# Kernel optimization log

Hardware: AMD Instinct MI355X
Metric: run time of the kernel (lower is better)

Reference implementation:

```python
import jax, jax.numpy as jnp
import numpy as np

B, T, S, E, H = 2, 2048, 2048, 1024, 16
DH = E // H

def setup_inputs() -> dict:
    key = jax.random.key(0)
    ks = jax.random.split(key, 12)
    sc = 1.0 / np.sqrt(E)
    inp = {
        'query': jax.random.normal(ks[0], (B, T, E), jnp.float32),
        'key':   jax.random.normal(ks[1], (B, S, E), jnp.float32),
        'value': jax.random.normal(ks[2], (B, S, E), jnp.float32),
        'Wq': jax.random.normal(ks[3], (E, E), jnp.float32) * sc,
        'bq': jnp.zeros((E,), jnp.float32),
        'Wk': jax.random.normal(ks[4], (E, E), jnp.float32) * sc,
        'bk': jnp.zeros((E,), jnp.float32),
        'Wv': jax.random.normal(ks[5], (E, E), jnp.float32) * sc,
        'bv': jnp.zeros((E,), jnp.float32),
        'Wo': jax.random.normal(ks[6], (E, E), jnp.float32) * sc,
        'bo': jnp.zeros((E,), jnp.float32),
    }
    return inp

def reference(query, key, value, Wq, bq, Wk, bk, Wv, bv, Wo, bo):
    # Linear projections (torch nn.Linear: x @ W.T + b)
    Q = query @ Wq.T + bq          # [B,T,E]
    K = key   @ Wk.T + bk          # [B,S,E]
    V = value @ Wv.T + bv          # [B,S,E]
    # split heads -> [B,H,L,DH]
    Q = Q.reshape(B, T, H, DH).transpose(0, 2, 1, 3)
    K = K.reshape(B, S, H, DH).transpose(0, 2, 1, 3)
    V = V.reshape(B, S, H, DH).transpose(0, 2, 1, 3)
    scores = jnp.einsum('bhtd,bhsd->bhts', Q, K) / jnp.sqrt(jnp.float32(DH))
    attn = jax.nn.softmax(scores, axis=-1)            # [B,H,T,S]
    out = jnp.einsum('bhts,bhsd->bhtd', attn, V)      # [B,H,T,DH]
    out = out.transpose(0, 2, 1, 3).reshape(B, T, E)
    out = out @ Wo.T + bo                             # [B,T,E]
    attn_avg = attn.mean(axis=1)                      # average_attn_weights=True
    return out, attn_avg
```

## Files before the change

kernel.cpp:

```cpp
#include <hip/hip_runtime.h>

#define DEV __device__ __forceinline__

typedef __attribute__((ext_vector_type(8))) short short8;
typedef __attribute__((ext_vector_type(4))) float floatx4;
typedef __attribute__((ext_vector_type(2))) unsigned int uint2v;
typedef unsigned short u16;

DEV u16 f2bf(float f) {
  unsigned int u = __float_as_uint(f);
  u += 0x7fffu + ((u >> 16) & 1u);
  return (u16)(u >> 16);
}

DEV unsigned int pk2bf(float a, float b) {
  unsigned int ua = __float_as_uint(a) + 0x8000u;
  unsigned int ub = __float_as_uint(b) + 0x8000u;
  return (ua >> 16) | (ub & 0xffff0000u);
}

DEV void load16_to_lds(const void* g, void* l) {
  __builtin_amdgcn_global_load_lds(
      (const __attribute__((address_space(1))) unsigned int*)g,
      (__attribute__((address_space(3))) unsigned int*)l, 16, 0, 0);
}

#define MFMA16(A, B, C) __builtin_amdgcn_mfma_f32_16x16x32_bf16(A, B, C, 0, 0, 0)

#define QSCALE 0.18033688011112042f

DEV void stage_block(const u16* src_row0, int k0, int ln, void* ldsbase) {
  int r = ln >> 2;
  int p = ((ln & 3) - (ln >> 4)) & 3;
  load16_to_lds((const char*)(src_row0 + (size_t)r * 1024 + k0) + p * 16, ldsbase);
}
DEV const short8* frag_addr(const u16* base, int blk, int c, int q) {
  int slot = c * 4 + ((q + (c >> 2)) & 3);
  return (const short8*)(base + blk * 512 + slot * 8);
}

__global__ __launch_bounds__(256) void cvt_all(
    const float* __restrict__ w0, const float* __restrict__ w1,
    const float* __restrict__ w2, const float* __restrict__ w3,
    const float* __restrict__ a0, const float* __restrict__ a1, const float* __restrict__ a2,
    u16* __restrict__ e0, u16* __restrict__ e1, u16* __restrict__ e2, u16* __restrict__ e3,
    u16* __restrict__ f0, u16* __restrict__ f1, u16* __restrict__ f2) {
  const int t = blockIdx.y;
  const float* s;
  u16* d;
  size_t base;
  if (t < 4) {
    s = t == 0 ? w0 : t == 1 ? w1 : t == 2 ? w2 : w3;
    d = t == 0 ? e0 : t == 1 ? e1 : t == 2 ? e2 : e3;
    base = 0;
  } else {
    int a = (t - 4) >> 2;
    s = a == 0 ? a0 : a == 1 ? a1 : a2;
    d = a == 0 ? f0 : a == 1 ? f1 : f2;
    base = (size_t)((t - 4) & 3) * 1048576;
  }
  size_t i = base + (size_t)(blockIdx.x * 256 + threadIdx.x) * 4;
  float4 v = *(const float4*)(s + i);
  ushort4 o;
  o.x = f2bf(v.x); o.y = f2bf(v.y); o.z = f2bf(v.z); o.w = f2bf(v.w);
  *(ushort4*)(d + i) = o;
}

__global__ __launch_bounds__(256) void qkv_gemm(
    const u16* __restrict__ qb, const u16* __restrict__ kb, const u16* __restrict__ vb,
    const u16* __restrict__ wq, const u16* __restrict__ wk, const u16* __restrict__ wv,
    const float* __restrict__ bq, const float* __restrict__ bk, const float* __restrict__ bv,
    u16* __restrict__ Qh, u16* __restrict__ Kh, u16* __restrict__ VT) {
  __shared__ __align__(16) u16 As[4096];
  __shared__ __align__(16) u16 Bs[4096];
  const int tid = threadIdx.x;
  const int w = tid >> 6, ln = tid & 63, q = ln >> 4, c = ln & 15;
  const int wr = w >> 1, wc = w & 1;
  const int z = blockIdx.z;
  const int m0 = (z == 2 ? blockIdx.x : blockIdx.y) * 128;
  const int n0 = (z == 2 ? blockIdx.y : blockIdx.x) * 128;
  const u16* Asrc = z == 0 ? qb : (z == 1 ? kb : wv);
  const u16* Bsrc = z == 0 ? wq : (z == 1 ? wk : vb);

  floatx4 acc[4][4];
#pragma unroll
  for (int i = 0; i < 4; ++i)
#pragma unroll
    for (int j = 0; j < 4; ++j) acc[i][j] = (floatx4){0.f, 0.f, 0.f, 0.f};

  for (int k0 = 0; k0 < 1024; k0 += 32) {
#pragma unroll
    for (int it = 0; it < 2; ++it) {
      int I = w * 2 + it;
      stage_block(Asrc + (size_t)(m0 + I * 16) * 1024, k0, ln, (char*)As + I * 1024);
      stage_block(Bsrc + (size_t)(n0 + I * 16) * 1024, k0, ln, (char*)Bs + I * 1024);
    }
    __syncthreads();
    short8 a[4], bb[4];
#pragma unroll
    for (int mt = 0; mt < 4; ++mt) a[mt] = *frag_addr(As, wr * 4 + mt, c, q);
#pragma unroll
    for (int nt = 0; nt < 4; ++nt) bb[nt] = *frag_addr(Bs, wc * 4 + nt, c, q);
#pragma unroll
    for (int mt = 0; mt < 4; ++mt)
#pragma unroll
      for (int nt = 0; nt < 4; ++nt) acc[mt][nt] = MFMA16(a[mt], bb[nt], acc[mt][nt]);
    __syncthreads();
  }

  if (z <= 1) {
    const float* bias = z ? bk : bq;
    u16* dst = z ? Kh : Qh;
    const float scale = z ? 1.0f : QSCALE;
    float bn[4];
#pragma unroll
    for (int nt = 0; nt < 4; ++nt) bn[nt] = bias[n0 + wc * 64 + nt * 16 + c];
#pragma unroll
    for (int mt = 0; mt < 4; ++mt)
#pragma unroll
      for (int r = 0; r < 4; ++r) {
        int m = m0 + wr * 64 + mt * 16 + 4 * q + r;
        int bbv = m >> 11, t = m & 2047;
#pragma unroll
        for (int nt = 0; nt < 4; ++nt) {
          int n = n0 + wc * 64 + nt * 16 + c;
          dst[((size_t)(bbv * 16 + (n >> 6)) * 2048 + t) * 64 + (n & 63)] =
              f2bf((acc[mt][nt][r] + bn[nt]) * scale);
        }
      }
  } else {
    float bm[4][4];
#pragma unroll
    for (int mt = 0; mt < 4; ++mt)
#pragma unroll
      for (int r = 0; r < 4; ++r) bm[mt][r] = bv[m0 + wr * 64 + mt * 16 + 4 * q + r];
#pragma unroll
    for (int mt = 0; mt < 4; ++mt)
#pragma unroll
      for (int r = 0; r < 4; ++r) {
        int d = m0 + wr * 64 + mt * 16 + 4 * q + r;
        int hh = d >> 6, dl = d & 63;
#pragma unroll
        for (int nt = 0; nt < 4; ++nt) {
          int s = n0 + wc * 64 + nt * 16 + c;
          int bbv = s >> 11, sl = s & 2047;
          VT[((size_t)(bbv * 16 + hh) * 64 + dl) * 2048 + sl] = f2bf(acc[mt][nt][r] + bm[mt][r]);
        }
      }
  }
}

__global__ __launch_bounds__(256) void oproj_gemm(const u16* __restrict__ Ap, const u16* __restrict__ Wp,
                                                  const float* __restrict__ bias, float* __restrict__ out) {
  __shared__ __align__(16) u16 As[4096];
  __shared__ __align__(16) u16 Bs[2048];
  const int tid = threadIdx.x;
  const int w = tid >> 6, ln = tid & 63, q = ln >> 4, c = ln & 15;
  const int wr = w >> 1, wc = w & 1;
  const int n0 = blockIdx.x * 64, m0 = blockIdx.y * 128;

  floatx4 acc[4][2];
#pragma unroll
  for (int i = 0; i < 4; ++i)
#pragma unroll
    for (int j = 0; j < 2; ++j) acc[i][j] = (floatx4){0.f, 0.f, 0.f, 0.f};

  for (int k0 = 0; k0 < 1024; k0 += 32) {
#pragma unroll
    for (int j = 0; j < 3; ++j) {
      int idx = w * 3 + j;
      if (idx < 8) {
        stage_block(Ap + (size_t)(m0 + idx * 16) * 1024, k0, ln, (char*)As + idx * 1024);
      } else {
        int bi = idx - 8;
        stage_block(Wp + (size_t)(n0 + bi * 16) * 1024, k0, ln, (char*)Bs + bi * 1024);
      }
    }
    __syncthreads();
    short8 a[4], bb[2];
#pragma unroll
    for (int mt = 0; mt < 4; ++mt) a[mt] = *frag_addr(As, wr * 4 + mt, c, q);
#pragma unroll
    for (int nt = 0; nt < 2; ++nt) bb[nt] = *frag_addr(Bs, wc * 2 + nt, c, q);
#pragma unroll
    for (int mt = 0; mt < 4; ++mt)
#pragma unroll
      for (int nt = 0; nt < 2; ++nt) acc[mt][nt] = MFMA16(a[mt], bb[nt], acc[mt][nt]);
    __syncthreads();
  }

  float bn[2];
#pragma unroll
  for (int nt = 0; nt < 2; ++nt) bn[nt] = bias[n0 + wc * 32 + nt * 16 + c];
#pragma unroll
  for (int mt = 0; mt < 4; ++mt)
#pragma unroll
    for (int r = 0; r < 4; ++r) {
      int m = m0 + wr * 64 + mt * 16 + 4 * q + r;
#pragma unroll
      for (int nt = 0; nt < 2; ++nt)
        out[(size_t)m * 1024 + n0 + wc * 32 + nt * 16 + c] = acc[mt][nt][r] + bn[nt];
    }
}

__global__ __launch_bounds__(256) void flash_attn(const u16* __restrict__ Qh, const u16* __restrict__ Kh,
                                                  const u16* __restrict__ VhT, u16* __restrict__ Obuf,
                                                  float* __restrict__ l_ws) {
  __shared__ __align__(16) u16 Ks[4096];
  __shared__ __align__(16) u16 VTs[4096];
  __shared__ __align__(16) u16 Ps[4][2][1152];
  const int tid = threadIdx.x;
  const int w = tid >> 6, ln = tid & 63, q = ln >> 4, c = ln & 15;
  const int t0 = blockIdx.x * 128, h = blockIdx.y, b = blockIdx.z;
  const size_t bh = (size_t)(b * 16 + h);
  const u16* Qbase = Qh + bh * 131072;
  const u16* Kbase = Kh + bh * 131072;
  const u16* Vbase = VhT + bh * 131072;

  short8 qf[2][2];
#pragma unroll
  for (int blk = 0; blk < 2; ++blk) {
    const u16* qr = Qbase + (size_t)(t0 + w * 32 + blk * 16 + c) * 64 + q * 8;
    qf[blk][0] = *(const short8*)qr;
    qf[blk][1] = *(const short8*)(qr + 32);
  }
  floatx4 oacc[2][4];
  float lacc[2] = {0.f, 0.f};
#pragma unroll
  for (int i = 0; i < 2; ++i)
#pragma unroll
    for (int j = 0; j < 4; ++j) oacc[i][j] = (floatx4){0.f, 0.f, 0.f, 0.f};

  const int srow = ln >> 3;
  const int sch = (ln & 7) ^ srow;
  const int cx = c & 7;

  for (int s0 = 0; s0 < 2048; s0 += 64) {
#pragma unroll
    for (int it = 0; it < 2; ++it) {
      int I = w * 2 + it;
      int row = I * 8 + srow;
      load16_to_lds((const char*)Kbase + ((size_t)(s0 + row) * 64 + sch * 8) * 2, (char*)Ks + I * 1024);
      load16_to_lds((const char*)Vbase + ((size_t)row * 2048 + s0 + sch * 8) * 2, (char*)VTs + I * 1024);
    }
    __syncthreads();
#pragma unroll
    for (int st = 0; st < 4; ++st) {
      const int row = st * 16 + c;
      short8 k0 = *(const short8*)(Ks + row * 64 + ((q ^ cx) << 3));
      short8 k1 = *(const short8*)(Ks + row * 64 + (((4 + q) ^ cx) << 3));
#pragma unroll
      for (int blk = 0; blk < 2; ++blk) {
        floatx4 zz = (floatx4){0.f, 0.f, 0.f, 0.f};
        zz = MFMA16(k0, qf[blk][0], zz);
        zz = MFMA16(k1, qf[blk][1], zz);
        float e0 = exp2f(zz[0]), e1 = exp2f(zz[1]), e2 = exp2f(zz[2]), e3 = exp2f(zz[3]);
        lacc[blk] += (e0 + e1) + (e2 + e3);
        uint2v pk = {pk2bf(e0, e1), pk2bf(e2, e3)};
        *(uint2v*)(&Ps[w][blk][c * 72 + st * 16 + 4 * q]) = pk;
      }
    }
    short8 pf[2][2];
#pragma unroll
    for (int blk = 0; blk < 2; ++blk) {
      pf[blk][0] = *(const short8*)(&Ps[w][blk][c * 72 + q * 8]);
      pf[blk][1] = *(const short8*)(&Ps[w][blk][c * 72 + 32 + q * 8]);
    }
#pragma unroll
    for (int dt = 0; dt < 4; ++dt) {
      const int row = dt * 16 + c;
      short8 v0 = *(const short8*)(VTs + row * 64 + ((q ^ cx) << 3));
      short8 v1 = *(const short8*)(VTs + row * 64 + (((4 + q) ^ cx) << 3));
#pragma unroll
      for (int blk = 0; blk < 2; ++blk) {
        oacc[blk][dt] = MFMA16(pf[blk][0], v0, oacc[blk][dt]);
        oacc[blk][dt] = MFMA16(pf[blk][1], v1, oacc[blk][dt]);
      }
    }
    __syncthreads();
  }
#pragma unroll
  for (int blk = 0; blk < 2; ++blk) {
    float v = lacc[blk];
    v += __shfl_xor(v, 16);
    v += __shfl_xor(v, 32);
    lacc[blk] = v;
    if (q == 0) l_ws[bh * 2048 + t0 + w * 32 + blk * 16 + c] = v;
  }
#pragma unroll
  for (int blk = 0; blk < 2; ++blk)
#pragma unroll
    for (int r = 0; r < 4; ++r) {
      float lv = __shfl(lacc[blk], 4 * q + r);
      float inv = __builtin_amdgcn_rcpf(lv);
      const int t = t0 + w * 32 + blk * 16 + 4 * q + r;
#pragma unroll
      for (int dt = 0; dt < 4; ++dt)
        Obuf[((size_t)b * 2048 + t) * 1024 + h * 64 + dt * 16 + c] = f2bf(oacc[blk][dt][r] * inv);
    }
}

__global__ __launch_bounds__(256) void attn_avg_k(const u16* __restrict__ Qh, const u16* __restrict__ Kh,
                                                  const float* __restrict__ l_ws, float* __restrict__ out2) {
  __shared__ __align__(16) u16 Ks[4096];
  const int tid = threadIdx.x;
  const int w = tid >> 6, ln = tid & 63, q = ln >> 4, c = ln & 15;
  const int s0 = blockIdx.x * 64, t0 = blockIdx.y * 128, b = blockIdx.z;
  const int srow = ln >> 3;
  const int sch = (ln & 7) ^ srow;
  const int cx = c & 7;

  floatx4 acc[2][4];
#pragma unroll
  for (int i = 0; i < 2; ++i)
#pragma unroll
    for (int j = 0; j < 4; ++j) acc[i][j] = (floatx4){0.f, 0.f, 0.f, 0.f};

  for (int h = 0; h < 16; ++h) {
    size_t bh = (size_t)(b * 16 + h);
    const u16* Kbase = Kh + bh * 131072;
#pragma unroll
    for (int it = 0; it < 2; ++it) {
      int I = w * 2 + it;
      int row = I * 8 + srow;
      load16_to_lds((const char*)Kbase + ((size_t)(s0 + row) * 64 + sch * 8) * 2, (char*)Ks + I * 1024);
    }
    short8 qf[2][2];
    float linv[2];
#pragma unroll
    for (int blk = 0; blk < 2; ++blk) {
      const u16* qr = Qh + bh * 131072 + (size_t)(t0 + w * 32 + blk * 16 + c) * 64 + q * 8;
      qf[blk][0] = *(const short8*)qr;
      qf[blk][1] = *(const short8*)(qr + 32);
      linv[blk] = __builtin_amdgcn_rcpf(l_ws[bh * 2048 + t0 + w * 32 + blk * 16 + c]) * 0.0625f;
    }
    __syncthreads();
#pragma unroll
    for (int st = 0; st < 4; ++st) {
      const int row = st * 16 + c;
      short8 k0 = *(const short8*)(Ks + row * 64 + ((q ^ cx) << 3));
      short8 k1 = *(const short8*)(Ks + row * 64 + (((4 + q) ^ cx) << 3));
#pragma unroll
      for (int blk = 0; blk < 2; ++blk) {
        floatx4 zz = (floatx4){0.f, 0.f, 0.f, 0.f};
        zz = MFMA16(k0, qf[blk][0], zz);
        zz = MFMA16(k1, qf[blk][1], zz);
#pragma unroll
        for (int r = 0; r < 4; ++r) acc[blk][st][r] += exp2f(zz[r]) * linv[blk];
      }
    }
    __syncthreads();
  }
#pragma unroll
  for (int blk = 0; blk < 2; ++blk) {
    const size_t t = (size_t)t0 + w * 32 + blk * 16 + c;
#pragma unroll
    for (int st = 0; st < 4; ++st) {
      float4 o;
      o.x = acc[blk][st][0]; o.y = acc[blk][st][1]; o.z = acc[blk][st][2]; o.w = acc[blk][st][3];
      *(float4*)(out2 + ((size_t)b * 2048 + t) * 2048 + s0 + st * 16 + 4 * q) = o;
    }
  }
}

extern "C" void kernel_launch(void* const* d_in, const int* in_sizes, int n_in,
                              void* d_out, int out_size, void* d_ws, size_t ws_size,
                              hipStream_t stream) {
  const float* query = (const float*)d_in[0];
  const float* key = (const float*)d_in[1];
  const float* value = (const float*)d_in[2];
  const float* Wq = (const float*)d_in[3];
  const float* bq = (const float*)d_in[4];
  const float* Wk = (const float*)d_in[5];
  const float* bk = (const float*)d_in[6];
  const float* Wv = (const float*)d_in[7];
  const float* bv = (const float*)d_in[8];
  const float* Wo = (const float*)d_in[9];
  const float* bo = (const float*)d_in[10];

  char* ws = (char*)d_ws;
  const size_t MB = 1024 * 1024;
  u16* wWq = (u16*)(ws + 0 * MB);
  u16* wWk = (u16*)(ws + 2 * MB);
  u16* wWv = (u16*)(ws + 4 * MB);
  u16* wWo = (u16*)(ws + 6 * MB);
  u16* wQh = (u16*)(ws + 8 * MB);
  u16* wKh = (u16*)(ws + 16 * MB);
  u16* wVT = (u16*)(ws + 24 * MB);
  u16* wO = (u16*)(ws + 32 * MB);
  float* wl = (float*)(ws + 40 * MB);
  float* out = (float*)d_out;
  float* out2 = out + (size_t)4194304;

  u16* qb = (u16*)out2;
  u16* kb = qb + 4194304;
  u16* vb = kb + 4194304;

  cvt_all<<<dim3(1024, 16), 256, 0, stream>>>(Wq, Wk, Wv, Wo, query, key, value,
                                              wWq, wWk, wWv, wWo, qb, kb, vb);
  qkv_gemm<<<dim3(8, 32, 3), 256, 0, stream>>>(qb, kb, vb, wWq, wWk, wWv,
                                               bq, bk, bv, wQh, wKh, wVT);
  flash_attn<<<dim3(16, 16, 2), 256, 0, stream>>>(wQh, wKh, wVT, wO, wl);
  attn_avg_k<<<dim3(32, 16, 2), 256, 0, stream>>>(wQh, wKh, wl, out2);
  oproj_gemm<<<dim3(16, 32), 256, 0, stream>>>(wO, wWo, bo, out);
}
```

Measured before the change: 323.9 us.

## Halve flash-attn query tile, double-buffer K in attn_avg, use native exp2

Flash attention now gives each wave 16 query rows instead of 32, so the grid doubles to 1024 blocks and occupancy rises. The cost is that each K/V tile loaded into LDS is reused by half as many rows. attn_avg_k double-buffers the per-head K tile so the next head's load overlaps the current head's compute, and it drops one barrier per iteration. Both kernels switch from exp2f to the hardware exp2 builtin, which skips the library's range handling.

After: 302.5 us. 1.07x faster.

```diff
diff --git a/kernel.cpp b/kernel.cpp
--- a/kernel.cpp
+++ b/kernel.cpp
@@ -26,6 +26,7 @@
 }
 
 #define MFMA16(A, B, C) __builtin_amdgcn_mfma_f32_16x16x32_bf16(A, B, C, 0, 0, 0)
+#define EXP2(x) __builtin_amdgcn_exp2f(x)
 
 #define QSCALE 0.18033688011112042f
 
@@ -208,28 +209,25 @@
                                                   float* __restrict__ l_ws) {
   __shared__ __align__(16) u16 Ks[4096];
   __shared__ __align__(16) u16 VTs[4096];
-  __shared__ __align__(16) u16 Ps[4][2][1152];
+  __shared__ __align__(16) u16 Ps[4][1152];
   const int tid = threadIdx.x;
   const int w = tid >> 6, ln = tid & 63, q = ln >> 4, c = ln & 15;
-  const int t0 = blockIdx.x * 128, h = blockIdx.y, b = blockIdx.z;
+  const int t0 = blockIdx.x * 64, h = blockIdx.y, b = blockIdx.z;
   const size_t bh = (size_t)(b * 16 + h);
   const u16* Qbase = Qh + bh * 131072;
   const u16* Kbase = Kh + bh * 131072;
   const u16* Vbase = VhT + bh * 131072;
 
-  short8 qf[2][2];
-#pragma unroll
-  for (int blk = 0; blk < 2; ++blk) {
-    const u16* qr = Qbase + (size_t)(t0 + w * 32 + blk * 16 + c) * 64 + q * 8;
-    qf[blk][0] = *(const short8*)qr;
-    qf[blk][1] = *(const short8*)(qr + 32);
-  }
-  floatx4 oacc[2][4];
-  float lacc[2] = {0.f, 0.f};
-#pragma unroll
-  for (int i = 0; i < 2; ++i)
-#pragma unroll
-    for (int j = 0; j < 4; ++j) oacc[i][j] = (floatx4){0.f, 0.f, 0.f, 0.f};
+  short8 qf0, qf1;
+  {
+    const u16* qr = Qbase + (size_t)(t0 + w * 16 + c) * 64 + q * 8;
+    qf0 = *(const short8*)qr;
+    qf1 = *(const short8*)(qr + 32);
+  }
+  floatx4 oacc[4];
+  float lacc = 0.f;
+#pragma unroll
+  for (int j = 0; j < 4; ++j) oacc[j] = (floatx4){0.f, 0.f, 0.f, 0.f};
 
   const int srow = ln >> 3;
   const int sch = (ln & 7) ^ srow;
@@ -249,60 +247,47 @@
       const int row = st * 16 + c;
       short8 k0 = *(const short8*)(Ks + row * 64 + ((q ^ cx) << 3));
       short8 k1 = *(const short8*)(Ks + row * 64 + (((4 + q) ^ cx) << 3));
-#pragma unroll
-      for (int blk = 0; blk < 2; ++blk) {
-        floatx4 zz = (floatx4){0.f, 0.f, 0.f, 0.f};
-        zz = MFMA16(k0, qf[blk][0], zz);
-        zz = MFMA16(k1, qf[blk][1], zz);
-        float e0 = exp2f(zz[0]), e1 = exp2f(zz[1]), e2 = exp2f(zz[2]), e3 = exp2f(zz[3]);
-        lacc[blk] += (e0 + e1) + (e2 + e3);
-        uint2v pk = {pk2bf(e0, e1), pk2bf(e2, e3)};
-        *(uint2v*)(&Ps[w][blk][c * 72 + st * 16 + 4 * q]) = pk;
-      }
-    }
-    short8 pf[2][2];
-#pragma unroll
-    for (int blk = 0; blk < 2; ++blk) {
-      pf[blk][0] = *(const short8*)(&Ps[w][blk][c * 72 + q * 8]);
-      pf[blk][1] = *(const short8*)(&Ps[w][blk][c * 72 + 32 + q * 8]);
-    }
+      floatx4 zz = (floatx4){0.f, 0.f, 0.f, 0.f};
+      zz = MFMA16(k0, qf0, zz);
+      zz = MFMA16(k1, qf1, zz);
+      float e0 = EXP2(zz[0]), e1 = EXP2(zz[1]), e2 = EXP2(zz[2]), e3 = EXP2(zz[3]);
+      lacc += (e0 + e1) + (e2 + e3);
+      uint2v pk = {pk2bf(e0, e1), pk2bf(e2, e3)};
+      *(uint2v*)(&Ps[w][c * 72 + st * 16 + 4 * q]) = pk;
+    }
+    short8 pf0 = *(const short8*)(&Ps[w][c * 72 + q * 8]);
+    short8 pf1 = *(const short8*)(&Ps[w][c * 72 + 32 + q * 8]);
 #pragma unroll
     for (int dt = 0; dt < 4; ++dt) {
       const int row = dt * 16 + c;
       short8 v0 = *(const short8*)(VTs + row * 64 + ((q ^ cx) << 3));
       short8 v1 = *(const short8*)(VTs + row * 64 + (((4 + q) ^ cx) << 3));
-#pragma unroll
-      for (int blk = 0; blk < 2; ++blk) {
-        oacc[blk][dt] = MFMA16(pf[blk][0], v0, oacc[blk][dt]);
-        oacc[blk][dt] = MFMA16(pf[blk][1], v1, oacc[blk][dt]);
-      }
-    }
-    __syncthreads();
-  }
-#pragma unroll
-  for (int blk = 0; blk < 2; ++blk) {
-    float v = lacc[blk];
+      oacc[dt] = MFMA16(pf0, v0, oacc[dt]);
+      oacc[dt] = MFMA16(pf1, v1, oacc[dt]);
+    }
+    __syncthreads();
+  }
+  {
+    float v = lacc;
     v += __shfl_xor(v, 16);
     v += __shfl_xor(v, 32);
-    lacc[blk] = v;
-    if (q == 0) l_ws[bh * 2048 + t0 + w * 32 + blk * 16 + c] = v;
-  }
-#pragma unroll
-  for (int blk = 0; blk < 2; ++blk)
-#pragma unroll
-    for (int r = 0; r < 4; ++r) {
-      float lv = __shfl(lacc[blk], 4 * q + r);
-      float inv = __builtin_amdgcn_rcpf(lv);
-      const int t = t0 + w * 32 + blk * 16 + 4 * q + r;
-#pragma unroll
-      for (int dt = 0; dt < 4; ++dt)
-        Obuf[((size_t)b * 2048 + t) * 1024 + h * 64 + dt * 16 + c] = f2bf(oacc[blk][dt][r] * inv);
-    }
+    lacc = v;
+    if (q == 0) l_ws[bh * 2048 + t0 + w * 16 + c] = v;
+  }
+#pragma unroll
+  for (int r = 0; r < 4; ++r) {
+    float lv = __shfl(lacc, 4 * q + r);
+    float inv = __builtin_amdgcn_rcpf(lv);
+    const int t = t0 + w * 16 + 4 * q + r;
+#pragma unroll
+    for (int dt = 0; dt < 4; ++dt)
+      Obuf[((size_t)b * 2048 + t) * 1024 + h * 64 + dt * 16 + c] = f2bf(oacc[dt][r] * inv);
+  }
 }
 
 __global__ __launch_bounds__(256) void attn_avg_k(const u16* __restrict__ Qh, const u16* __restrict__ Kh,
                                                   const float* __restrict__ l_ws, float* __restrict__ out2) {
-  __shared__ __align__(16) u16 Ks[4096];
+  __shared__ __align__(16) u16 Ks[2][4096];
   const int tid = threadIdx.x;
   const int w = tid >> 6, ln = tid & 63, q = ln >> 4, c = ln & 15;
   const int s0 = blockIdx.x * 64, t0 = blockIdx.y * 128, b = blockIdx.z;
@@ -316,14 +301,27 @@
 #pragma unroll
     for (int j = 0; j < 4; ++j) acc[i][j] = (floatx4){0.f, 0.f, 0.f, 0.f};
 
+#pragma unroll
+  for (int it = 0; it < 2; ++it) {
+    int I = w * 2 + it;
+    int row = I * 8 + srow;
+    load16_to_lds((const char*)(Kh + (size_t)(b * 16) * 131072) + ((size_t)(s0 + row) * 64 + sch * 8) * 2,
+                  (char*)Ks[0] + I * 1024);
+  }
+
   for (int h = 0; h < 16; ++h) {
-    size_t bh = (size_t)(b * 16 + h);
-    const u16* Kbase = Kh + bh * 131072;
-#pragma unroll
-    for (int it = 0; it < 2; ++it) {
-      int I = w * 2 + it;
-      int row = I * 8 + srow;
-      load16_to_lds((const char*)Kbase + ((size_t)(s0 + row) * 64 + sch * 8) * 2, (char*)Ks + I * 1024);
+    const size_t bh = (size_t)(b * 16 + h);
+    const u16* ks = Ks[h & 1];
+    __syncthreads();
+    if (h < 15) {
+      const u16* Kn = Kh + (bh + 1) * 131072;
+#pragma unroll
+      for (int it = 0; it < 2; ++it) {
+        int I = w * 2 + it;
+        int row = I * 8 + srow;
+        load16_to_lds((const char*)Kn + ((size_t)(s0 + row) * 64 + sch * 8) * 2,
+                      (char*)Ks[(h + 1) & 1] + I * 1024);
+      }
     }
     short8 qf[2][2];
     float linv[2];
@@ -334,22 +332,20 @@
       qf[blk][1] = *(const short8*)(qr + 32);
       linv[blk] = __builtin_amdgcn_rcpf(l_ws[bh * 2048 + t0 + w * 32 + blk * 16 + c]) * 0.0625f;
     }
-    __syncthreads();
 #pragma unroll
     for (int st = 0; st < 4; ++st) {
       const int row = st * 16 + c;
-      short8 k0 = *(const short8*)(Ks + row * 64 + ((q ^ cx) << 3));
-      short8 k1 = *(const short8*)(Ks + row * 64 + (((4 + q) ^ cx) << 3));
+      short8 k0 = *(const short8*)(ks + row * 64 + ((q ^ cx) << 3));
+      short8 k1 = *(const short8*)(ks + row * 64 + (((4 + q) ^ cx) << 3));
 #pragma unroll
       for (int blk = 0; blk < 2; ++blk) {
         floatx4 zz = (floatx4){0.f, 0.f, 0.f, 0.f};
         zz = MFMA16(k0, qf[blk][0], zz);
         zz = MFMA16(k1, qf[blk][1], zz);
 #pragma unroll
-        for (int r = 0; r < 4; ++r) acc[blk][st][r] += exp2f(zz[r]) * linv[blk];
+        for (int r = 0; r < 4; ++r) acc[blk][st][r] += EXP2(zz[r]) * linv[blk];
       }
     }
-    __syncthreads();
   }
 #pragma unroll
   for (int blk = 0; blk < 2; ++blk) {
@@ -400,7 +396,7 @@
                                               wWq, wWk, wWv, wWo, qb, kb, vb);
   qkv_gemm<<<dim3(8, 32, 3), 256, 0, stream>>>(qb, kb, vb, wWq, wWk, wWv,
                                                bq, bk, bv, wQh, wKh, wVT);
-  flash_attn<<<dim3(16, 16, 2), 256, 0, stream>>>(wQh, wKh, wVT, wO, wl);
+  flash_attn<<<dim3(32, 16, 2), 256, 0, stream>>>(wQh, wKh, wVT, wO, wl);
   attn_avg_k<<<dim3(32, 16, 2), 256, 0, stream>>>(wQh, wKh, wl, out2);
   oproj_gemm<<<dim3(16, 32), 256, 0, stream>>>(wO, wWo, bo, out);
 }
```
